# Performance work log

Measured on AMD Instinct MI355X. Metric: run time of the kernel, lower is better.

Reference implementation:

```python
import jax, jax.numpy as jnp
import numpy as np

B, L, D_MODEL = 4, 2048, 768
EXPAND, D_STATE, D_CONV = 2, 16, 4
D_INNER = EXPAND * D_MODEL
DT_RANK = (D_MODEL + 15) // 16  # ceil(d_model/16) = 48


def setup_inputs() -> dict:
    key = jax.random.key(0)
    ks = jax.random.split(key, 8)
    s = lambda n: 1.0 / np.sqrt(n)
    hidden_states = jax.random.normal(ks[0], (B, L, D_MODEL), jnp.float32)
    in_proj_w = jax.random.normal(ks[1], (2 * D_INNER, D_MODEL), jnp.float32) * s(D_MODEL)
    conv_w = jax.random.normal(ks[2], (D_INNER, 1, D_CONV), jnp.float32) * s(D_CONV)
    conv_b = jax.random.normal(ks[3], (D_INNER,), jnp.float32) * 0.05
    x_proj_w = jax.random.normal(ks[4], (DT_RANK + 2 * D_STATE, D_INNER), jnp.float32) * s(D_INNER)
    dt_proj_w = jax.random.uniform(ks[5], (D_INNER, DT_RANK), jnp.float32,
                                   -DT_RANK ** -0.5, DT_RANK ** -0.5)
    # dt bias init: inverse-softplus of dt sampled log-uniform in [1e-3, 1e-1]
    dt = jnp.exp(jax.random.uniform(ks[6], (D_INNER,), jnp.float32)
                 * (np.log(0.1) - np.log(0.001)) + np.log(0.001))
    dt = jnp.clip(dt, 1e-4)
    dt_proj_b = dt + jnp.log(-jnp.expm1(-dt))
    A_log = jnp.log(jnp.broadcast_to(jnp.arange(1, D_STATE + 1, dtype=jnp.float32),
                                     (D_INNER, D_STATE)))
    D_param = jnp.ones((D_INNER,), jnp.float32)
    out_proj_w = jax.random.normal(ks[7], (D_MODEL, D_INNER), jnp.float32) * s(D_INNER)
    return dict(hidden_states=hidden_states, in_proj_w=in_proj_w, conv_w=conv_w,
                conv_b=conv_b, x_proj_w=x_proj_w, dt_proj_w=dt_proj_w,
                dt_proj_b=dt_proj_b, A_log=A_log, D_param=D_param,
                out_proj_w=out_proj_w)


def _selective_scan(u, delta, A, Bmat, Cmat):
    # u, delta: [B,L,Di]; A: [Di,N]; Bmat, Cmat: [B,L,N]
    u_t = jnp.swapaxes(u, 0, 1)        # [L,B,Di]
    d_t = jnp.swapaxes(delta, 0, 1)    # [L,B,Di]
    B_t = jnp.swapaxes(Bmat, 0, 1)     # [L,B,N]
    C_t = jnp.swapaxes(Cmat, 0, 1)     # [L,B,N]

    def step(h, inp):
        u_i, d_i, b_i, c_i = inp
        dA = jnp.exp(d_i[:, :, None] * A[None])                  # [B,Di,N]
        dBu = d_i[:, :, None] * b_i[:, None, :] * u_i[:, :, None]
        h = h * dA + dBu
        y = jnp.einsum('bdn,bn->bd', h, c_i)
        return h, y

    h0 = jnp.zeros((u.shape[0], A.shape[0], A.shape[1]), u.dtype)
    _, ys = jax.lax.scan(step, h0, (u_t, d_t, B_t, C_t))
    return jnp.swapaxes(ys, 0, 1)      # [B,L,Di]


def reference(hidden_states, in_proj_w, conv_w, conv_b, x_proj_w,
              dt_proj_w, dt_proj_b, A_log, D_param, out_proj_w):
    xz = jnp.einsum('bld,ed->ble', hidden_states, in_proj_w)     # [B,L,2*Di]
    x, z = jnp.split(xz, 2, axis=-1)

    # causal depthwise conv1d (left-pad d_conv-1) + SiLU
    x_ncl = jnp.swapaxes(x, 1, 2)                                # [B,Di,L]
    x_conv = jax.lax.conv_general_dilated(
        x_ncl, conv_w, window_strides=(1,), padding=[(D_CONV - 1, 0)],
        dimension_numbers=('NCH', 'OIH', 'NCH'),
        feature_group_count=D_INNER) + conv_b[None, :, None]
    x = jax.nn.silu(jnp.swapaxes(x_conv, 1, 2))                  # [B,L,Di]

    x_dbl = jnp.einsum('bld,ed->ble', x, x_proj_w)               # [B,L,dt_rank+2N]
    dt, Bmat, Cmat = jnp.split(x_dbl, [DT_RANK, DT_RANK + D_STATE], axis=-1)
    delta = jax.nn.softplus(jnp.einsum('blr,dr->bld', dt, dt_proj_w)
                            + dt_proj_b)                         # [B,L,Di]
    A = -jnp.exp(A_log)                                          # [Di,N]

    y = _selective_scan(x, delta, A, Bmat, Cmat)
    y = y + x * D_param
    y = y * jax.nn.silu(z)
    return jnp.einsum('bld,od->blo', y, out_proj_w)              # [B,L,D_model]
```

## Files before the change

kernel.cpp:

```cpp
#include <hip/hip_runtime.h>
#include <hip/hip_bf16.h>


#define NB 4
#define LL 2048
#define DM 768
#define DI 1536
#define NST 16
#define DTR 48
#define XPR 80
#define CHUNKS 32
#define CLEN 64
#define LOG2E 1.442695040888963f

typedef __attribute__((ext_vector_type(4))) float f32x4;
typedef __attribute__((ext_vector_type(8))) short s16x8;
typedef __attribute__((ext_vector_type(8))) unsigned short u16x8;

__device__ __forceinline__ void store_c(float* p, float v) { *p = v; }
__device__ __forceinline__ void store_c(__hip_bfloat16* p, float v)
{ *p = __float2bfloat16(v); }

__device__ __forceinline__ float bf2f(unsigned short u)
{
    union { unsigned int i; float f; } c; c.i = ((unsigned int)u) << 16;
    return c.f;
}
__device__ __forceinline__ unsigned short f2bf(float f)
{
    union { __hip_bfloat16 h; unsigned short u; } c;
    c.h = __float2bfloat16(f);
    return c.u;
}

__device__ __forceinline__ void pow_chain(float p, float* dA)
{
    dA[0] = p;
#pragma unroll
    for (int n = 1; n < NST; ++n) {
        const int a = (n + 1) >> 1, b = (n + 1) - a;
        dA[n] = dA[a - 1] * dA[b - 1];
    }
}

__device__ __forceinline__ void gload16(const __hip_bfloat16* g, char* l)
{
    __builtin_amdgcn_global_load_lds(
        (const __attribute__((address_space(1))) void*)g,
        (__attribute__((address_space(3))) void*)l, 16, 0, 0);
}

__global__ __launch_bounds__(256) void cast_bf16(
    const float* __restrict__ in, __hip_bfloat16* __restrict__ out, int n4)
{
    const int i = blockIdx.x * 256 + threadIdx.x;
    if (i >= n4) return;
    const float4 v = ((const float4*)in)[i];
    union { ushort4 u; __hip_bfloat16 h[4]; } o;
    o.h[0] = __float2bfloat16(v.x);
    o.h[1] = __float2bfloat16(v.y);
    o.h[2] = __float2bfloat16(v.z);
    o.h[3] = __float2bfloat16(v.w);
    ((ushort4*)out)[i] = o.u;
}

__global__ __launch_bounds__(256) void cast_pad_rows(
    const float* __restrict__ in, __hip_bfloat16* __restrict__ out,
    int rows_in, int rows_out, int cols)
{
    const int i = blockIdx.x * 256 + threadIdx.x;
    const int total = rows_out * cols / 4;
    if (i >= total) return;
    const int row = (i * 4) / cols;
    union { ushort4 u; __hip_bfloat16 h[4]; } o;
    if (row < rows_in) {
        const float4 v = ((const float4*)in)[i];
        o.h[0] = __float2bfloat16(v.x);
        o.h[1] = __float2bfloat16(v.y);
        o.h[2] = __float2bfloat16(v.z);
        o.h[3] = __float2bfloat16(v.w);
    } else {
        o.h[0] = o.h[1] = o.h[2] = o.h[3] = __float2bfloat16(0.f);
    }
    ((ushort4*)out)[i] = o.u;
}

__global__ __launch_bounds__(256) void cast_pad_cols(
    const float* __restrict__ in, __hip_bfloat16* __restrict__ out,
    int cols_in, int cols_out, int rows)
{
    const int i = blockIdx.x * 256 + threadIdx.x;
    if (i >= rows * cols_out) return;
    const int row = i / cols_out, col = i - row * cols_out;
    out[i] = __float2bfloat16(col < cols_in ? in[row * cols_in + col] : 0.f);
}

template <typename CT>
__global__ __launch_bounds__(512, 2) void gemm_bf16_256(
    const __hip_bfloat16* __restrict__ A, int lda,
    const __hip_bfloat16* __restrict__ W, int ldw,
    CT* __restrict__ C, int ldc, int K)
{
    __shared__ __align__(16) char lds[131072];

    const int tid = threadIdx.x;
    const int w = tid >> 6, lane = tid & 63;
    const int wm = w >> 2, wn = w & 3;
    const int l15 = lane & 15, l4 = lane >> 4;
    const int m0 = blockIdx.y * 256, n0 = blockIdx.x * 256;

    const int r0 = tid >> 2, r1 = r0 + 128;
    const int k8 = ((tid & 3) ^ ((r0 >> 1) & 3)) << 3;
    const __hip_bfloat16* Ab = A + (size_t)m0 * lda;
    const __hip_bfloat16* Wb = W + (size_t)n0 * ldw;
    const size_t aoff0 = (size_t)r0 * lda + k8, aoff1 = (size_t)r1 * lda + k8;
    const size_t woff0 = (size_t)r0 * ldw + k8, woff1 = (size_t)r1 * ldw + k8;

    const int NK = K >> 6;
    const int NH = NK << 2;

    const int sw = (l4 ^ ((l15 >> 1) & 3)) << 4;
    int aoff[8], boff[4];
#pragma unroll
    for (int f = 0; f < 8; ++f)
        aoff[f] = ((wm * 128 + f * 16 + l15) << 6) + sw;
#pragma unroll
    for (int n = 0; n < 4; ++n)
        boff[n] = ((wn * 64 + n * 16 + l15) << 6) + sw;

    auto stage = [&](int s) {
        const int kt2 = s >> 2, which = s & 3;
        const int kofs = (kt2 << 6) + (((s >> 1) & 1) << 5);
        char* l0 = &lds[((kt2 & 1) << 16) + (which << 14) + (w << 10)];
        if (which & 1) {
            gload16(Ab + aoff0 + kofs, l0);
            gload16(Ab + aoff1 + kofs, l0 + 8192);
        } else {
            gload16(Wb + woff0 + kofs, l0);
            gload16(Wb + woff1 + kofs, l0 + 8192);
        }
    };

    for (int s = 0; s < 7; ++s) stage(s);
    asm volatile("s_waitcnt vmcnt(6)" ::: "memory");
    asm volatile("s_barrier" ::: "memory");

    f32x4 acc[8][4] = {};
    s16x8 a[4], b[4];
    int sQ = 7;

#define PH_MFMA(MB)                                                        \
    __builtin_amdgcn_s_setprio(1);                                         \
    _Pragma("unroll")                                                      \
    for (int f = 0; f < 4; ++f)                                            \
        _Pragma("unroll")                                                  \
        for (int n = 0; n < 4; ++n)                                        \
            acc[(MB) + f][n] = __builtin_amdgcn_mfma_f32_16x16x32_bf16(    \
                a[f], b[n], acc[(MB) + f][n], 0, 0, 0);                    \
    __builtin_amdgcn_s_setprio(0);

    for (int kt = 0; kt < NK; ++kt) {
        const int rb = (kt & 1) << 16;
#pragma unroll
        for (int f = 0; f < 4; ++f) a[f] = *(const s16x8*)&lds[rb + 16384 + aoff[f]];
#pragma unroll
        for (int n = 0; n < 4; ++n) b[n] = *(const s16x8*)&lds[rb + boff[n]];
        if (sQ < NH) stage(sQ);
        ++sQ;
        asm volatile("s_barrier" ::: "memory");
        PH_MFMA(0)
        asm volatile("s_barrier" ::: "memory");
#pragma unroll
        for (int f = 0; f < 4; ++f) a[f] = *(const s16x8*)&lds[rb + 16384 + aoff[4 + f]];
        if (sQ < NH) stage(sQ);
        ++sQ;
        asm volatile("s_barrier" ::: "memory");
        PH_MFMA(4)
        asm volatile("s_barrier" ::: "memory");
#pragma unroll
        for (int f = 0; f < 4; ++f) a[f] = *(const s16x8*)&lds[rb + 49152 + aoff[f]];
#pragma unroll
        for (int n = 0; n < 4; ++n) b[n] = *(const s16x8*)&lds[rb + 32768 + boff[n]];
        if (sQ < NH) stage(sQ);
        ++sQ;
        asm volatile("s_barrier" ::: "memory");
        PH_MFMA(0)
        asm volatile("s_barrier" ::: "memory");
#pragma unroll
        for (int f = 0; f < 4; ++f) a[f] = *(const s16x8*)&lds[rb + 49152 + aoff[4 + f]];
        if (sQ < NH) stage(sQ);
        ++sQ;
        asm volatile("s_barrier" ::: "memory");
        PH_MFMA(4)
        asm volatile("s_waitcnt vmcnt(6)" ::: "memory");
        asm volatile("s_barrier" ::: "memory");
    }
#undef PH_MFMA

#pragma unroll
    for (int f = 0; f < 8; ++f)
#pragma unroll
        for (int r = 0; r < 4; ++r) {
            const size_t row = (size_t)(m0 + wm * 128 + f * 16 + l4 * 4 + r);
#pragma unroll
            for (int n = 0; n < 4; ++n)
                store_c(&C[row * ldc + n0 + wn * 64 + n * 16 + l15], acc[f][n][r]);
        }
}

template <int EPI, typename CT>
__global__ __launch_bounds__(256) void gemm_bf16(
    const __hip_bfloat16* __restrict__ A, int lda,
    const __hip_bfloat16* __restrict__ W, int ldw,
    CT* __restrict__ C, int ldc, int K,
    const float* __restrict__ bias, __hip_bfloat16* __restrict__ aux)
{
    __shared__ __align__(16) char lds[2][16384];

    const int tid  = threadIdx.x;
    const int wv   = tid >> 6;
    const int lane = tid & 63;
    const int m0 = blockIdx.y * 128;
    const int n0 = blockIdx.x * 128;
    const int wr = (wv >> 1) * 64;
    const int wc = (wv & 1) * 64;
    const int l15 = lane & 15;
    const int l4  = lane >> 4;

    const int c0 = wv * 2, c1 = wv * 2 + 1;
    const int i0 = c0 * 64 + lane, i1 = c1 * 64 + lane;
    const int ks0 = i0 >> 7, ro0 = i0 & 127;
    const int ks1 = i1 >> 7, ro1 = i1 & 127;

    const __hip_bfloat16* Ag0 = A + (size_t)(m0 + ro0) * lda + ks0 * 8;
    const __hip_bfloat16* Ag1 = A + (size_t)(m0 + ro1) * lda + ks1 * 8;
    const __hip_bfloat16* Wg0 = W + (size_t)(n0 + ro0) * ldw + ks0 * 8;
    const __hip_bfloat16* Wg1 = W + (size_t)(n0 + ro1) * ldw + ks1 * 8;

    f32x4 acc[4][4] = {};

    const int nt = K >> 5;

    {
        char* dst = lds[0];
        gload16(Ag0, dst + c0 * 1024);
        gload16(Ag1, dst + c1 * 1024);
        gload16(Wg0, dst + 8192 + c0 * 1024);
        gload16(Wg1, dst + 8192 + c1 * 1024);
    }
    __syncthreads();

    for (int t = 0; t < nt; ++t) {
        const int cur = t & 1;
        if (t + 1 < nt) {
            const int k0 = (t + 1) << 5;
            char* dst = lds[cur ^ 1];
            gload16(Ag0 + k0, dst + c0 * 1024);
            gload16(Ag1 + k0, dst + c1 * 1024);
            gload16(Wg0 + k0, dst + 8192 + c0 * 1024);
            gload16(Wg1 + k0, dst + 8192 + c1 * 1024);
        }
        const char* bufA = lds[cur];
        const char* bufB = lds[cur] + 8192;
        s16x8 af[4], bfr[4];
#pragma unroll
        for (int i = 0; i < 4; ++i)
            af[i] = *(const s16x8*)(bufA + ((l4 * 128 + wr + i * 16 + l15) << 4));
#pragma unroll
        for (int j = 0; j < 4; ++j)
            bfr[j] = *(const s16x8*)(bufB + ((l4 * 128 + wc + j * 16 + l15) << 4));
#pragma unroll
        for (int i = 0; i < 4; ++i)
#pragma unroll
            for (int j = 0; j < 4; ++j)
                acc[i][j] = __builtin_amdgcn_mfma_f32_16x16x32_bf16(
                    af[i], bfr[j], acc[i][j], 0, 0, 0);
        __syncthreads();
    }

#pragma unroll
    for (int i = 0; i < 4; ++i)
#pragma unroll
        for (int r = 0; r < 4; ++r) {
            const size_t row = (size_t)(m0 + wr + i * 16 + l4 * 4 + r);
#pragma unroll
            for (int j = 0; j < 4; ++j) {
                const int col = wc + j * 16 + l15;
                const float v = acc[i][j][r];
                if (EPI == 0) {
                    store_c(&C[row * ldc + n0 + col], v);
                } else if (EPI == 1) {
                    const float x = v + bias[n0 + col];
                    store_c(&C[row * ldc + n0 + col],
                            fmaxf(x, 0.f) + log1pf(expf(-fabsf(x))));
                } else {
                    if (col < XPR) store_c(&C[row * ldc + col], v);
                    if (col < 64)  aux[row * 64 + col] = __float2bfloat16(v);
                }
            }
        }
}

__global__ __launch_bounds__(256) void conv_silu(
    const __hip_bfloat16* __restrict__ xz, const float* __restrict__ cw,
    const float* __restrict__ cb, __hip_bfloat16* __restrict__ xc)
{
    const int nd8 = DI / 8;
    const int idx = blockIdx.x * 256 + threadIdx.x;
    if (idx >= NB * LL * nd8) return;
    const int d8 = idx % nd8;
    const int bl = idx / nd8;
    const int l = bl % LL;
    const int b = bl / LL;
    const int d = d8 * 8;

    const __hip_bfloat16* xrow = xz + ((size_t)b * LL) * (2 * DI) + d;
    float x[4][8];
#pragma unroll
    for (int j = 0; j < 4; ++j) {
        const int ll = l - 3 + j;
        if (ll >= 0) {
            const u16x8 v = *(const u16x8*)(xrow + (size_t)ll * (2 * DI));
#pragma unroll
            for (int k = 0; k < 8; ++k) x[j][k] = bf2f(v[k]);
        } else {
#pragma unroll
            for (int k = 0; k < 8; ++k) x[j][k] = 0.f;
        }
    }
    union { u16x8 v; unsigned short u[8]; } o;
#pragma unroll
    for (int k = 0; k < 8; ++k) {
        const float4 w = *(const float4*)(cw + (d + k) * 4);
        float acc = cb[d + k];
        acc = fmaf(w.x, x[0][k], acc);
        acc = fmaf(w.y, x[1][k], acc);
        acc = fmaf(w.z, x[2][k], acc);
        acc = fmaf(w.w, x[3][k], acc);
        const float s = acc * __builtin_amdgcn_rcpf(1.f + __expf(-acc));
        o.u[k] = f2bf(s);
    }
    *(u16x8*)(xc + (size_t)bl * DI + d) = o.v;
}

__global__ __launch_bounds__(256) void scan_phase1(
    const __hip_bfloat16* __restrict__ u, const __hip_bfloat16* __restrict__ delta,
    const float* __restrict__ xdbl,
    float* __restrict__ hend, float* __restrict__ sumdv)
{
    __shared__ float Bs[CLEN][NST];
    const int t = threadIdx.x;
    const int d = blockIdx.x * 256 + t;
    const int c = blockIdx.y;
    const int b = blockIdx.z;
    const size_t row0 = (size_t)b * LL + c * CLEN;

    for (int e = t; e < CLEN * NST; e += 256) {
        const int r = e >> 4, col = e & 15;
        Bs[r][col] = xdbl[(row0 + r) * XPR + DTR + col];
    }
    __syncthreads();

    float h[NST] = {};
    float sdv = 0.f;
    const __hip_bfloat16* dp = delta + row0 * DI + d;
    const __hip_bfloat16* up = u + row0 * DI + d;
    for (int l = 0; l < CLEN; ++l) {
        const float dv = __bfloat162float(dp[(size_t)l * DI]);
        const float uv = __bfloat162float(up[(size_t)l * DI]);
        sdv += dv;
        const float du = dv * uv;
        float dA[NST];
        pow_chain(__builtin_amdgcn_exp2f(-dv * LOG2E), dA);
#pragma unroll
        for (int n = 0; n < NST; ++n)
            h[n] = fmaf(h[n], dA[n], du * Bs[l][n]);
    }
#pragma unroll
    for (int n = 0; n < NST; ++n)
        hend[(((size_t)b * CHUNKS + c) * NST + n) * DI + d] = h[n];
    sumdv[((size_t)b * CHUNKS + c) * DI + d] = sdv;
}

__global__ __launch_bounds__(256) void scan_phase2(
    const float* __restrict__ hend, const float* __restrict__ sumdv,
    float* __restrict__ hin)
{
    const int idx = blockIdx.x * 256 + threadIdx.x;
    const int d = idx % DI;
    const int n = (idx / DI) & (NST - 1);
    const int b = idx / (DI * NST);
    const float A2 = -(float)(n + 1) * LOG2E;
    float h = 0.f;
    for (int c = 0; c < CHUNKS; ++c) {
        const size_t base = (size_t)b * CHUNKS + c;
        hin[(base * NST + n) * DI + d] = h;
        const float P = __builtin_amdgcn_exp2f(sumdv[base * DI + d] * A2);
        h = fmaf(h, P, hend[(base * NST + n) * DI + d]);
    }
}

__global__ __launch_bounds__(256) void scan_phase3(
    const __hip_bfloat16* __restrict__ u, const __hip_bfloat16* __restrict__ delta_in,
    const float* __restrict__ xdbl,
    const float* __restrict__ Dp, const __hip_bfloat16* __restrict__ xz,
    const float* __restrict__ hin, __hip_bfloat16* __restrict__ ybf)
{
    __shared__ float BCs[CLEN][2 * NST];
    const int t = threadIdx.x;
    const int d = blockIdx.x * 256 + t;
    const int c = blockIdx.y;
    const int b = blockIdx.z;
    const size_t row0 = (size_t)b * LL + c * CLEN;

    for (int e = t; e < CLEN * 2 * NST; e += 256) {
        const int r = e >> 5, col = e & 31;
        BCs[r][col] = xdbl[(row0 + r) * XPR + DTR + col];
    }
    __syncthreads();

    float h[NST];
#pragma unroll
    for (int n = 0; n < NST; ++n)
        h[n] = hin[(((size_t)b * CHUNKS + c) * NST + n) * DI + d];

    const float Dv = Dp[d];
    const __hip_bfloat16* dp = delta_in + row0 * DI + d;
    const __hip_bfloat16* up = u + row0 * DI + d;
    const __hip_bfloat16* zp = xz + row0 * (2 * DI) + DI + d;
    __hip_bfloat16* yp = ybf + row0 * (2 * DI) + d;

    for (int l = 0; l < CLEN; ++l) {
        const float dv = __bfloat162float(dp[(size_t)l * DI]);
        const float uv = __bfloat162float(up[(size_t)l * DI]);
        const float zv = __bfloat162float(zp[(size_t)l * 2 * DI]);
        const float du = dv * uv;
        float dA[NST];
        pow_chain(__builtin_amdgcn_exp2f(-dv * LOG2E), dA);
        float yv = 0.f;
#pragma unroll
        for (int n = 0; n < NST; ++n)
            h[n] = fmaf(h[n], dA[n], du * BCs[l][n]);
#pragma unroll
        for (int n = 0; n < NST; ++n)
            yv = fmaf(h[n], BCs[l][NST + n], yv);
        const float sz = zv * __builtin_amdgcn_rcpf(1.f + __expf(-zv));
        yp[(size_t)l * 2 * DI] = __float2bfloat16((yv + uv * Dv) * sz);
    }
}

extern "C" void kernel_launch(void* const* d_in, const int* in_sizes, int n_in,
                              void* d_out, int out_size, void* d_ws, size_t ws_size,
                              hipStream_t stream)
{
    const float* hidden     = (const float*)d_in[0];
    const float* in_proj_w  = (const float*)d_in[1];
    const float* conv_w     = (const float*)d_in[2];
    const float* conv_b     = (const float*)d_in[3];
    const float* x_proj_w   = (const float*)d_in[4];
    const float* dt_proj_w  = (const float*)d_in[5];
    const float* dt_proj_b  = (const float*)d_in[6];
    const float* A_log      = (const float*)d_in[7];
    const float* D_param    = (const float*)d_in[8];
    const float* out_proj_w = (const float*)d_in[9];
    float* out = (float*)d_out;
    (void)A_log;

    float* ws = (float*)d_ws;
    __hip_bfloat16* xzbf    = (__hip_bfloat16*)ws;
    __hip_bfloat16* xcbf    = (__hip_bfloat16*)(ws + 12582912);
    float*          xdbl    = ws + 18874368;
    __hip_bfloat16* deltabf = (__hip_bfloat16*)(ws + 19529728);
    float*          hend    = ws + 25821184;
    float*          hin     = ws + 28966912;
    float*          sumdv   = ws + 32112640;
    __hip_bfloat16* hidden_bf = (__hip_bfloat16*)(ws + 32309248);
    __hip_bfloat16* inw_bf    = (__hip_bfloat16*)(ws + 35454976);
    __hip_bfloat16* outw_bf   = (__hip_bfloat16*)(ws + 36634624);
    __hip_bfloat16* xdbl_bf   = (__hip_bfloat16*)(ws + 37224448);
    __hip_bfloat16* xpw_bf    = (__hip_bfloat16*)(ws + 37486592);
    __hip_bfloat16* dtw_bf    = (__hip_bfloat16*)(ws + 37584896);

    const int M = NB * LL;

    cast_bf16<<<(6291456 / 4 + 255) / 256, 256, 0, stream>>>(hidden, hidden_bf, 6291456 / 4);
    cast_bf16<<<(2359296 / 4 + 255) / 256, 256, 0, stream>>>(in_proj_w, inw_bf, 2359296 / 4);
    cast_bf16<<<(1179648 / 4 + 255) / 256, 256, 0, stream>>>(out_proj_w, outw_bf, 1179648 / 4);
    cast_pad_rows<<<(128 * 1536 / 4 + 255) / 256, 256, 0, stream>>>(
        x_proj_w, xpw_bf, XPR, 128, 1536);
    cast_pad_cols<<<(1536 * 64 + 255) / 256, 256, 0, stream>>>(
        dt_proj_w, dtw_bf, DTR, 64, 1536);

    gemm_bf16_256<__hip_bfloat16><<<dim3((2 * DI) / 256, M / 256), 512, 0, stream>>>(
        hidden_bf, DM, inw_bf, DM, xzbf, 2 * DI, DM);

    conv_silu<<<(M * (DI / 8) + 255) / 256, 256, 0, stream>>>(
        xzbf, conv_w, conv_b, xcbf);

    gemm_bf16<2, float><<<dim3(1, M / 128), 256, 0, stream>>>(
        xcbf, DI, xpw_bf, DI, xdbl, XPR, DI, nullptr, xdbl_bf);

    gemm_bf16<1, __hip_bfloat16><<<dim3(DI / 128, M / 128), 256, 0, stream>>>(
        xdbl_bf, 64, dtw_bf, 64, deltabf, DI, 64, dt_proj_b, nullptr);

    dim3 gscan(DI / 256, CHUNKS, NB);
    scan_phase1<<<gscan, 256, 0, stream>>>(xcbf, deltabf, xdbl, hend, sumdv);
    scan_phase2<<<(NB * NST * DI) / 256, 256, 0, stream>>>(hend, sumdv, hin);
    scan_phase3<<<gscan, 256, 0, stream>>>(xcbf, deltabf, xdbl, D_param,
                                           xzbf, hin, xzbf);

    gemm_bf16_256<float><<<dim3(DM / 256, M / 256), 512, 0, stream>>>(
        xzbf, 2 * DI, outw_bf, DI, out, DM, DI);
}
```

Before: 308.3 us.

## Split-K the x_proj and out_proj GEMMs and merge cast kernels

Fuses the five weight/input cast kernels into one launch. The x_proj GEMM, which previously launched only 64 blocks, is split four ways along K into partial buffers, and a new combine kernel sums them and writes both the fp32 and bf16 outputs. The out_proj GEMM, which previously launched 96 blocks, is split two ways along K with a final add kernel. The aim is to fill more compute units on these undersized GEMMs, at the cost of extra partial-sum memory traffic and two additional launches.

```diff
diff --git a/kernel.cpp b/kernel.cpp
--- a/kernel.cpp
+++ b/kernel.cpp
@@ -32,74 +32,85 @@
     c.h = __float2bfloat16(f);
     return c.u;
 }
-
-__device__ __forceinline__ void pow_chain(float p, float* dA)
-{
-    dA[0] = p;
-#pragma unroll
-    for (int n = 1; n < NST; ++n) {
-        const int a = (n + 1) >> 1, b = (n + 1) - a;
-        dA[n] = dA[a - 1] * dA[b - 1];
-    }
-}
-
-__device__ __forceinline__ void gload16(const __hip_bfloat16* g, char* l)
-{
-    __builtin_amdgcn_global_load_lds(
-        (const __attribute__((address_space(1))) void*)g,
-        (__attribute__((address_space(3))) void*)l, 16, 0, 0);
-}
-
-__global__ __launch_bounds__(256) void cast_bf16(
-    const float* __restrict__ in, __hip_bfloat16* __restrict__ out, int n4)
-{
-    const int i = blockIdx.x * 256 + threadIdx.x;
-    if (i >= n4) return;
-    const float4 v = ((const float4*)in)[i];
+__device__ __forceinline__ ushort4 cvt4(float4 v)
+{
     union { ushort4 u; __hip_bfloat16 h[4]; } o;
     o.h[0] = __float2bfloat16(v.x);
     o.h[1] = __float2bfloat16(v.y);
     o.h[2] = __float2bfloat16(v.z);
     o.h[3] = __float2bfloat16(v.w);
-    ((ushort4*)out)[i] = o.u;
-}
-
-__global__ __launch_bounds__(256) void cast_pad_rows(
-    const float* __restrict__ in, __hip_bfloat16* __restrict__ out,
-    int rows_in, int rows_out, int cols)
-{
-    const int i = blockIdx.x * 256 + threadIdx.x;
-    const int total = rows_out * cols / 4;
-    if (i >= total) return;
-    const int row = (i * 4) / cols;
-    union { ushort4 u; __hip_bfloat16 h[4]; } o;
-    if (row < rows_in) {
-        const float4 v = ((const float4*)in)[i];
-        o.h[0] = __float2bfloat16(v.x);
-        o.h[1] = __float2bfloat16(v.y);
-        o.h[2] = __float2bfloat16(v.z);
-        o.h[3] = __float2bfloat16(v.w);
-    } else {
-        o.h[0] = o.h[1] = o.h[2] = o.h[3] = __float2bfloat16(0.f);
-    }
-    ((ushort4*)out)[i] = o.u;
-}
-
-__global__ __launch_bounds__(256) void cast_pad_cols(
-    const float* __restrict__ in, __hip_bfloat16* __restrict__ out,
-    int cols_in, int cols_out, int rows)
-{
-    const int i = blockIdx.x * 256 + threadIdx.x;
-    if (i >= rows * cols_out) return;
-    const int row = i / cols_out, col = i - row * cols_out;
-    out[i] = __float2bfloat16(col < cols_in ? in[row * cols_in + col] : 0.f);
+    return o.u;
+}
+
+__device__ __forceinline__ void pow_chain(float p, float* dA)
+{
+    dA[0] = p;
+#pragma unroll
+    for (int n = 1; n < NST; ++n) {
+        const int a = (n + 1) >> 1, b = (n + 1) - a;
+        dA[n] = dA[a - 1] * dA[b - 1];
+    }
+}
+
+__device__ __forceinline__ void gload16(const __hip_bfloat16* g, char* l)
+{
+    __builtin_amdgcn_global_load_lds(
+        (const __attribute__((address_space(1))) void*)g,
+        (__attribute__((address_space(3))) void*)l, 16, 0, 0);
+}
+
+#define CS0 1572864
+#define CS1 589824
+#define CS2 294912
+#define CS3 49152
+#define CS4 24576
+#define CTOT (CS0 + CS1 + CS2 + CS3 + CS4)
+
+__global__ __launch_bounds__(256) void cast_all(
+    const float* __restrict__ hidden, const float* __restrict__ inw,
+    const float* __restrict__ outw, const float* __restrict__ xpw,
+    const float* __restrict__ dtw,
+    __hip_bfloat16* __restrict__ o_hidden, __hip_bfloat16* __restrict__ o_inw,
+    __hip_bfloat16* __restrict__ o_outw, __hip_bfloat16* __restrict__ o_xpw,
+    __hip_bfloat16* __restrict__ o_dtw)
+{
+    int i = blockIdx.x * 256 + threadIdx.x;
+    if (i >= CTOT) return;
+    if (i < CS0) {
+        ((ushort4*)o_hidden)[i] = cvt4(((const float4*)hidden)[i]);
+        return;
+    }
+    i -= CS0;
+    if (i < CS1) {
+        ((ushort4*)o_inw)[i] = cvt4(((const float4*)inw)[i]);
+        return;
+    }
+    i -= CS1;
+    if (i < CS2) {
+        ((ushort4*)o_outw)[i] = cvt4(((const float4*)outw)[i]);
+        return;
+    }
+    i -= CS2;
+    if (i < CS3) {
+        float4 v = make_float4(0.f, 0.f, 0.f, 0.f);
+        if (i < (XPR * DI) / 4) v = ((const float4*)xpw)[i];
+        ((ushort4*)o_xpw)[i] = cvt4(v);
+        return;
+    }
+    i -= CS3;
+    {
+        const int e = i * 4, row = e >> 6, col = e & 63;
+        float4 v = make_float4(0.f, 0.f, 0.f, 0.f);
+        if (col < DTR) v = *(const float4*)(dtw + row * DTR + col);
+        ((ushort4*)o_dtw)[i] = cvt4(v);
+    }
 }
 
 template <typename CT>
 __global__ __launch_bounds__(512, 2) void gemm_bf16_256(
     const __hip_bfloat16* __restrict__ A, int lda,
     const __hip_bfloat16* __restrict__ W, int ldw,
-    CT* __restrict__ C, int ldc, int K)
+    CT* __restrict__ C, int ldc, int K, size_t cstride)
 {
     __shared__ __align__(16) char lds[131072];
 
@@ -108,6 +119,10 @@
     const int wm = w >> 2, wn = w & 3;
     const int l15 = lane & 15, l4 = lane >> 4;
     const int m0 = blockIdx.y * 256, n0 = blockIdx.x * 256;
+    const int z = blockIdx.z;
+    A += (size_t)z * K;
+    W += (size_t)z * K;
+    C += (size_t)z * cstride;
 
     const int r0 = tid >> 2, r1 = r0 + 128;
     const int k8 = ((tid & 3) ^ ((r0 >> 1) & 3)) << 3;
@@ -213,7 +228,7 @@
     const __hip_bfloat16* __restrict__ A, int lda,
     const __hip_bfloat16* __restrict__ W, int ldw,
     CT* __restrict__ C, int ldc, int K,
-    const float* __restrict__ bias, __hip_bfloat16* __restrict__ aux)
+    const float* __restrict__ bias)
 {
     __shared__ __align__(16) char lds[2][16384];
 
@@ -226,6 +241,13 @@
     const int wc = (wv & 1) * 64;
     const int l15 = lane & 15;
     const int l4  = lane >> 4;
+
+    if (EPI == 3) {
+        const int z = blockIdx.z;
+        A += (size_t)z * K;
+        W += (size_t)z * K;
+        C += (size_t)z * 8192 * XPR;
+    }
 
     const int c0 = wv * 2, c1 = wv * 2 + 1;
     const int i0 = c0 * 64 + lane, i1 = c1 * 64 + lane;
@@ -287,18 +309,41 @@
             for (int j = 0; j < 4; ++j) {
                 const int col = wc + j * 16 + l15;
                 const float v = acc[i][j][r];
-                if (EPI == 0) {
-                    store_c(&C[row * ldc + n0 + col], v);
-                } else if (EPI == 1) {
+                if (EPI == 1) {
                     const float x = v + bias[n0 + col];
                     store_c(&C[row * ldc + n0 + col],
                             fmaxf(x, 0.f) + log1pf(expf(-fabsf(x))));
+                } else if (EPI == 3) {
+                    if (col < XPR) C[row * XPR + col] = v;
                 } else {
-                    if (col < XPR) store_c(&C[row * ldc + col], v);
-                    if (col < 64)  aux[row * 64 + col] = __float2bfloat16(v);
+                    store_c(&C[row * ldc + n0 + col], v);
                 }
             }
         }
+}
+
+__global__ __launch_bounds__(256) void x_combine(
+    const float* __restrict__ xpart, float* __restrict__ xdbl,
+    __hip_bfloat16* __restrict__ xdbl_bf)
+{
+    const int i = blockIdx.x * 256 + threadIdx.x;
+    if (i >= 8192 * XPR) return;
+    float s = xpart[i] + xpart[655360 + i] + xpart[2 * 655360 + i]
+            + xpart[3 * 655360 + i];
+    xdbl[i] = s;
+    const int r = i / XPR, c = i - r * XPR;
+    if (c < 64) xdbl_bf[r * 64 + c] = __float2bfloat16(s);
+}
+
+__global__ __launch_bounds__(256) void o_add(
+    const float* __restrict__ p0, const float* __restrict__ p1,
+    float* __restrict__ out)
+{
+    const int i = blockIdx.x * 256 + threadIdx.x;
+    if (i >= (8192 * DM) / 4) return;
+    const float4 a = ((const float4*)p0)[i];
+    const float4 b = ((const float4*)p1)[i];
+    ((float4*)out)[i] = make_float4(a.x + b.x, a.y + b.y, a.z + b.z, a.w + b.w);
 }
 
 __global__ __launch_bounds__(256) void conv_silu(
@@ -481,27 +526,28 @@
     __hip_bfloat16* xpw_bf    = (__hip_bfloat16*)(ws + 37486592);
     __hip_bfloat16* dtw_bf    = (__hip_bfloat16*)(ws + 37584896);
 
+    float* xpart  = ws + 25821184;
+    float* opart0 = ws + 12582912;
+    float* opart1 = ws + 19529728;
+
     const int M = NB * LL;
 
-    cast_bf16<<<(6291456 / 4 + 255) / 256, 256, 0, stream>>>(hidden, hidden_bf, 6291456 / 4);
-    cast_bf16<<<(2359296 / 4 + 255) / 256, 256, 0, stream>>>(in_proj_w, inw_bf, 2359296 / 4);
-    cast_bf16<<<(1179648 / 4 + 255) / 256, 256, 0, stream>>>(out_proj_w, outw_bf, 1179648 / 4);
-    cast_pad_rows<<<(128 * 1536 / 4 + 255) / 256, 256, 0, stream>>>(
-        x_proj_w, xpw_bf, XPR, 128, 1536);
-    cast_pad_cols<<<(1536 * 64 + 255) / 256, 256, 0, stream>>>(
-        dt_proj_w, dtw_bf, DTR, 64, 1536);
-
-    gemm_bf16_256<__hip_bfloat16><<<dim3((2 * DI) / 256, M / 256), 512, 0, stream>>>(
-        hidden_bf, DM, inw_bf, DM, xzbf, 2 * DI, DM);
+    cast_all<<<(CTOT + 255) / 256, 256, 0, stream>>>(
+        hidden, in_proj_w, out_proj_w, x_proj_w, dt_proj_w,
+        hidden_bf, inw_bf, outw_bf, xpw_bf, dtw_bf);
+
+    gemm_bf16_256<__hip_bfloat16><<<dim3((2 * DI) / 256, M / 256, 1), 512, 0, stream>>>(
+        hidden_bf, DM, inw_bf, DM, xzbf, 2 * DI, DM, 0);
 
     conv_silu<<<(M * (DI / 8) + 255) / 256, 256, 0, stream>>>(
         xzbf, conv_w, conv_b, xcbf);
 
-    gemm_bf16<2, float><<<dim3(1, M / 128), 256, 0, stream>>>(
-        xcbf, DI, xpw_bf, DI, xdbl, XPR, DI, nullptr, xdbl_bf);
-
-    gemm_bf16<1, __hip_bfloat16><<<dim3(DI / 128, M / 128), 256, 0, stream>>>(
-        xdbl_bf, 64, dtw_bf, 64, deltabf, DI, 64, dt_proj_b, nullptr);
+    gemm_bf16<3, float><<<dim3(1, M / 128, 4), 256, 0, stream>>>(
+        xcbf, DI, xpw_bf, DI, xpart, XPR, DI / 4, nullptr);
+    x_combine<<<(8192 * XPR + 255) / 256, 256, 0, stream>>>(xpart, xdbl, xdbl_bf);
+
+    gemm_bf16<1, __hip_bfloat16><<<dim3(DI / 128, M / 128, 1), 256, 0, stream>>>(
+        xdbl_bf, 64, dtw_bf, 64, deltabf, DI, 64, dt_proj_b);
 
     dim3 gscan(DI / 256, CHUNKS, NB);
     scan_phase1<<<gscan, 256, 0, stream>>>(xcbf, deltabf, xdbl, hend, sumdv);
@@ -509,6 +555,8 @@
     scan_phase3<<<gscan, 256, 0, stream>>>(xcbf, deltabf, xdbl, D_param,
                                            xzbf, hin, xzbf);
 
-    gemm_bf16_256<float><<<dim3(DM / 256, M / 256), 512, 0, stream>>>(
-        xzbf, 2 * DI, outw_bf, DI, out, DM, DI);
-}
+    gemm_bf16_256<float><<<dim3(DM / 256, M / 256, 2), 512, 0, stream>>>(
+        xzbf, 2 * DI, outw_bf, DI, opart0, DM, DI / 2,
+        (size_t)(opart1 - opart0));
+    o_add<<<(8192 * DM / 4 + 255) / 256, 256, 0, stream>>>(opart0, opart1, out);
+}
```

Measured after the change: 276.1 us. -10.5%, faster.
